# Performance work log

Measured on AMD Instinct MI355X. Metric: run time of the kernel, lower is better.

Reference implementation:

```python
import jax, jax.numpy as jnp
import numpy as np

D_MODEL = 2048
N_HEADS = 16
N_KV_HEADS = 4
HEAD_DIM = D_MODEL // N_HEADS  # 128
SWA_WINDOW = 1024
SINK_TOKENS = 4
ROPE_BASE = 10000.0
EPS = 1e-6


def setup_inputs() -> dict:
    key = jax.random.key(0)
    ks = jax.random.split(key, 6)
    s = 0.02
    B, T = 1, 4096
    return {
        "x": jax.random.normal(ks[0], (B, T, D_MODEL), dtype=jnp.float32),
        "wq": jax.random.normal(ks[1], (N_HEADS * HEAD_DIM, D_MODEL), dtype=jnp.float32) * s,
        "wk": jax.random.normal(ks[2], (N_KV_HEADS * HEAD_DIM, D_MODEL), dtype=jnp.float32) * s,
        "wv": jax.random.normal(ks[3], (N_KV_HEADS * HEAD_DIM, D_MODEL), dtype=jnp.float32) * s,
        "wo": jax.random.normal(ks[4], (D_MODEL, D_MODEL), dtype=jnp.float32) * s,
        "qk_weight": jnp.ones((HEAD_DIM,), dtype=jnp.float32),
        "layer_idx": 1,
    }


def _rope_cos_sin(T, dtype):
    half = HEAD_DIM // 2
    inv_freq = 1.0 / (ROPE_BASE ** (jnp.arange(half, dtype=dtype) / half))
    freqs = jnp.arange(T, dtype=dtype)[:, None] * inv_freq[None, :]  # [T, half]
    return jnp.cos(freqs), jnp.sin(freqs)


def _rot(x, cos, sin):
    # x: [B,H,T,D]; cos/sin: [T,D/2]
    half = HEAD_DIM // 2
    x1, x2 = x[..., :half], x[..., half:]
    return jnp.concatenate([x1 * cos - x2 * sin, x1 * sin + x2 * cos], axis=-1)


def _qknorm(x, w):
    rms = jnp.sqrt(jnp.mean(x * x, axis=-1, keepdims=True) + EPS)
    return x / rms * w


def reference(x, wq, wk, wv, wo, qk_weight, layer_idx):
    B, T, C = x.shape
    rep = N_HEADS // N_KV_HEADS
    q = (x @ wq.T).reshape(B, T, N_HEADS, HEAD_DIM).transpose(0, 2, 1, 3)      # [B,H,T,D]
    k = (x @ wk.T).reshape(B, T, N_KV_HEADS, HEAD_DIM).transpose(0, 2, 1, 3)   # [B,Hkv,T,D]
    v = (x @ wv.T).reshape(B, T, N_KV_HEADS, HEAD_DIM).transpose(0, 2, 1, 3)
    k = jnp.repeat(k, rep, axis=1)  # GQA expand, matches repeat_interleave
    v = jnp.repeat(v, rep, axis=1)

    cos, sin = _rope_cos_sin(T, x.dtype)
    q = _rot(q, cos, sin)
    k = _rot(k, cos, sin)

    q = _qknorm(q, qk_weight)
    k = _qknorm(k, qk_weight)

    # sliding-window + sink mask (non-global layer). NOTE: faithful to the
    # original, which passes ~allowed as the boolean keep-mask to SDPA.
    i = jnp.arange(T)[:, None]
    j = jnp.arange(T)[None, :]
    allowed = (j <= i) & (((i - j) < SWA_WINDOW) | (j < SINK_TOKENS))
    keep = ~allowed  # True = attend (SDPA bool-mask semantics)

    scale = HEAD_DIM ** -0.5
    scores = jnp.einsum('bhqd,bhkd->bhqk', q, k) * scale
    scores = jnp.where(keep[None, None], scores, -jnp.inf)
    attn = jax.nn.softmax(scores, axis=-1)
    y = jnp.einsum('bhqk,bhkd->bhqd', attn, v)
    y = y.transpose(0, 2, 1, 3).reshape(B, T, C)
    return y @ wo.T
```

## Files before the change

kernel.cpp:

```cpp
#include <hip/hip_runtime.h>

typedef unsigned short u16;
typedef __bf16 bf16x8_t __attribute__((ext_vector_type(8)));
typedef float f32x4 __attribute__((ext_vector_type(4)));
typedef u16 u16x8 __attribute__((ext_vector_type(8)));
typedef u16 u16x4 __attribute__((ext_vector_type(4)));

__device__ __forceinline__ u16 f2bf(float f) {
  union { float f; unsigned u; } v; v.f = f;
  unsigned r = v.u + 0x7FFFu + ((v.u >> 16) & 1u);
  return (u16)(r >> 16);
}
__device__ __forceinline__ float bf2f(u16 b) {
  union { unsigned u; float f; } v; v.u = ((unsigned)b) << 16;
  return v.f;
}
__device__ __forceinline__ f32x4 mfma_bf16(u16x8 a, u16x8 b, f32x4 c) {
  return __builtin_amdgcn_mfma_f32_16x16x32_bf16(
      __builtin_bit_cast(bf16x8_t, a), __builtin_bit_cast(bf16x8_t, b), c, 0, 0, 0);
}
__device__ __forceinline__ unsigned pack_bf16_trunc(float a, float b) {
  return __builtin_amdgcn_perm(__builtin_bit_cast(unsigned, b),
                               __builtin_bit_cast(unsigned, a), 0x07060302u);
}

__global__ void k_cvt_all(const float* __restrict__ x,  const float* __restrict__ wq,
                          const float* __restrict__ wk, const float* __restrict__ wv,
                          const float* __restrict__ wo, u16* __restrict__ xb,
                          u16* __restrict__ wqkvb, u16* __restrict__ wob) {
  const int i = blockIdx.x * blockDim.x + threadIdx.x;
  const float* src;
  u16* dst;
  int off;
  if (i < 2097152)      { src = x;  dst = xb;               off = i; }
  else if (i < 3145728) { src = wq; dst = wqkvb;            off = i - 2097152; }
  else if (i < 3407872) { src = wk; dst = wqkvb + 4194304;  off = i - 3145728; }
  else if (i < 3670016) { src = wv; dst = wqkvb + 5242880;  off = i - 3407872; }
  else                  { src = wo; dst = wob;              off = i - 3670016; }
  float4 v = reinterpret_cast<const float4*>(src)[off];
  u16x4 o = { f2bf(v.x), f2bf(v.y), f2bf(v.z), f2bf(v.w) };
  reinterpret_cast<u16x4*>(dst)[off] = o;
}

template<bool BF16OUT>
__global__ __launch_bounds__(256, 2)
void k_gemm_bt(const u16* __restrict__ A, const u16* __restrict__ B,
               void* __restrict__ Cv, int M, int N, int K) {
  __shared__ u16 lA[128 * 64];
  __shared__ u16 lB[128 * 64];
  const int bm = blockIdx.y, bn = blockIdx.x;
  const int tid = threadIdx.x;
  const int wid = tid >> 6, lane = tid & 63;
  const int lo = lane & 15, hi = lane >> 4;
  const int wrow = (wid >> 1) * 64, wcol = (wid & 1) * 64;
  f32x4 acc[4][4] = {};
  const size_t abase = (size_t)(bm * 128) * K;
  const size_t bbase = (size_t)(bn * 128) * K;
  for (int kt = 0; kt < K; kt += 64) {
#pragma unroll
    for (int rr = 0; rr < 4; ++rr) {
      int e = (rr * 256 + tid) * 8;
      int row = e >> 6, col = e & 63;
      u16x8 va = *reinterpret_cast<const u16x8*>(A + abase + (size_t)row * K + kt + col);
      u16x8 vb = *reinterpret_cast<const u16x8*>(B + bbase + (size_t)row * K + kt + col);
      int sw = ((row * 64 + col) * 2) ^ ((row & 7) << 4);
      *reinterpret_cast<u16x8*>(reinterpret_cast<char*>(lA) + sw) = va;
      *reinterpret_cast<u16x8*>(reinterpret_cast<char*>(lB) + sw) = vb;
    }
    __syncthreads();
#pragma unroll
    for (int ks = 0; ks < 64; ks += 32) {
      u16x8 af[4], bfr[4];
#pragma unroll
      for (int mi = 0; mi < 4; ++mi) {
        int row = wrow + mi * 16 + lo, col = ks + hi * 8;
        int sw = ((row * 64 + col) * 2) ^ ((row & 7) << 4);
        af[mi] = *reinterpret_cast<const u16x8*>(reinterpret_cast<char*>(lA) + sw);
      }
#pragma unroll
      for (int ni = 0; ni < 4; ++ni) {
        int row = wcol + ni * 16 + lo, col = ks + hi * 8;
        int sw = ((row * 64 + col) * 2) ^ ((row & 7) << 4);
        bfr[ni] = *reinterpret_cast<const u16x8*>(reinterpret_cast<char*>(lB) + sw);
      }
#pragma unroll
      for (int mi = 0; mi < 4; ++mi)
#pragma unroll
        for (int ni = 0; ni < 4; ++ni)
          acc[mi][ni] = mfma_bf16(af[mi], bfr[ni], acc[mi][ni]);
    }
    __syncthreads();
  }
#pragma unroll
  for (int mi = 0; mi < 4; ++mi)
#pragma unroll
    for (int ni = 0; ni < 4; ++ni)
#pragma unroll
      for (int r = 0; r < 4; ++r) {
        int row = bm * 128 + wrow + mi * 16 + hi * 4 + r;
        int col = bn * 128 + wcol + ni * 16 + lo;
        if (BF16OUT)
          ((u16*)Cv)[(size_t)row * N + col] = f2bf(acc[mi][ni][r]);
        else
          ((float*)Cv)[(size_t)row * N + col] = acc[mi][ni][r];
      }
}

#define ATT_SL2E 0.12754276432973518f
__global__ void k_rope_norm(const u16* __restrict__ QKV, const float* __restrict__ qkw,
                            u16* __restrict__ qb, u16* __restrict__ kb) {
  int gw = blockIdx.x * 4 + (threadIdx.x >> 6);
  int lane = threadIdx.x & 63;
  int t = gw / 20, hh = gw - t * 20;
  const u16* src = QKV + (size_t)t * 3072 + (hh < 16 ? hh * 128 : 2048 + (hh - 16) * 128);
  float x1 = bf2f(src[lane]), x2 = bf2f(src[lane + 64]);
  float invf = exp2f(-(float)lane * (13.287712379549449f / 64.0f));
  float fr = (float)t * invf;
  float sn, cs;
  sincosf(fr, &sn, &cs);
  float o1 = x1 * cs - x2 * sn, o2 = x1 * sn + x2 * cs;
  float ss = o1 * o1 + o2 * o2;
#pragma unroll
  for (int off = 32; off > 0; off >>= 1) ss += __shfl_xor(ss, off);
  float inv = rsqrtf(ss * (1.0f / 128.0f) + 1e-6f);
  inv *= (hh < 16) ? ATT_SL2E : 1.0f;
  o1 *= inv * qkw[lane];
  o2 *= inv * qkw[lane + 64];
  u16* dst = (hh < 16) ? (qb + ((size_t)hh * 4096 + t) * 128)
                       : (kb + ((size_t)(hh - 16) * 4096 + t) * 128);
  dst[lane] = f2bf(o1);
  dst[lane + 64] = f2bf(o2);
}

__global__ void k_transpose_v(const u16* __restrict__ QKV, u16* __restrict__ vtb) {
  __shared__ float lt[64][65];
  int b = blockIdx.x;
  int dt = b & 1, tt = (b >> 1) & 63, kv = b >> 7;
  int tid = threadIdx.x;
#pragma unroll
  for (int rr = 0; rr < 16; ++rr) {
    int row = rr * 4 + (tid >> 6);
    int col = tid & 63;
    lt[row][col] = bf2f(QKV[(size_t)(tt * 64 + row) * 3072 + 2560 + kv * 128 + dt * 64 + col]);
  }
  __syncthreads();
#pragma unroll
  for (int pp = 0; pp < 2; ++pp) {
    int idx = pp * 256 + tid;
    int dr = idx >> 3, tc = (idx & 7) * 8;
    const int grp = tc >> 5;
    const int pb = tc & 31;
    u16x8 o;
#pragma unroll
    for (int i = 0; i < 8; ++i) {
      const int p = pb + i;
      const int g = (p & 3) | (((p >> 3) & 3) << 2) | (((p >> 2) & 1) << 4);
      o[i] = f2bf(lt[grp * 32 + g][dr]);
    }
    *reinterpret_cast<u16x8*>(vtb + (size_t)(kv * 128 + dt * 64 + dr) * 4096 + tt * 64 + tc) = o;
  }
}

#define KPAD 136
#define VPAD 40

__global__ __launch_bounds__(256)
void k_attn_mfma(const u16* __restrict__ qb, const u16* __restrict__ kb,
                 const u16* __restrict__ vtb, u16* __restrict__ yb) {
  __shared__ u16 sK[2][32][KPAD];
  __shared__ u16 sV[2][128][VPAD];
  const int id = blockIdx.x;
  const int work = (id & 7) * 64 + (id >> 3);
  const int kvh = work >> 7;
  const int rem = work & 127;
  const int h = kvh * 4 + (rem >> 5);
  const int qt = rem & 31;
  const int tid = threadIdx.x;
  const int wid = tid >> 6, lane = tid & 63;
  const int lo = lane & 15, hi = lane >> 4;
  const int q0 = qt * 128;
  const int qwA = q0 + wid * 16;
  const int qwB = qwA + 64;
  const int qrowA = qwA + lo, qrowB = qwB + lo;
  const u16* qpA = qb + ((size_t)h * 4096 + qrowA) * 128;
  const u16* qpB = qb + ((size_t)h * 4096 + qrowB) * 128;
  u16x8 qfA[4], qfB[4];
#pragma unroll
  for (int dc = 0; dc < 4; ++dc) {
    qfA[dc] = *reinterpret_cast<const u16x8*>(qpA + dc * 32 + hi * 8);
    qfB[dc] = *reinterpret_cast<const u16x8*>(qpB + dc * 32 + hi * 8);
  }
  f32x4 accOA[8] = {}, accOB[8] = {};
  float lsA = 0.0f, lsB = 0.0f;
  const u16* kbase = kb + (size_t)kvh * 4096 * 128;
  const u16* vb = vtb + (size_t)kvh * 128 * 4096;

  int past_tiles = 0;
  const int pe = q0 + 127 - 1024;
  if (pe >= 4) past_tiles = (pe >> 5) + 1;
  const int fstart = (q0 + 1) >> 5;
  const int ntiles = past_tiles + (128 - fstart);
  const int safe_past_hi = (q0 >= 1056) ? ((q0 - 1055) >> 5) : 0;
  const int funmask = (q0 >> 5) + 4;

  u16x8 kr[2], vr[2];
#define STAGE_LOAD(KT)                                                          \
  {                                                                             \
    const int kt_ = (KT);                                                       \
    _Pragma("unroll")                                                           \
    for (int p = 0; p < 2; ++p) {                                               \
      const int c = tid + p * 256;                                              \
      kr[p] = *reinterpret_cast<const u16x8*>(                                  \
          kbase + (size_t)(kt_ * 32 + (c >> 4)) * 128 + (c & 15) * 8);          \
      vr[p] = *reinterpret_cast<const u16x8*>(                                  \
          vb + (size_t)(c >> 2) * 4096 + kt_ * 32 + (c & 3) * 8);               \
    }                                                                           \
  }
#define STAGE_WRITE(BUF)                                                        \
  {                                                                             \
    const int b_ = (BUF);                                                       \
    _Pragma("unroll")                                                           \
    for (int p = 0; p < 2; ++p) {                                               \
      const int c = tid + p * 256;                                              \
      *reinterpret_cast<u16x8*>(&sK[b_][c >> 4][(c & 15) * 8]) = kr[p];         \
      *reinterpret_cast<u16x8*>(&sV[b_][c >> 2][(c & 3) * 8]) = vr[p];          \
    }                                                                           \
  }
#define COMPUTE(MSK)                                                            \
  {                                                                             \
    f32x4 aSA[2] = {}, aSB[2] = {};                                             \
    __builtin_amdgcn_s_setprio(1);                                              \
    _Pragma("unroll")                                                           \
    for (int sub = 0; sub < 2; ++sub)                                           \
      _Pragma("unroll")                                                         \
      for (int dc = 0; dc < 4; ++dc) {                                          \
        u16x8 kf = *reinterpret_cast<const u16x8*>(                             \
            &sK[cur][sub * 16 + lo][dc * 32 + hi * 8]);                         \
        aSA[sub] = mfma_bf16(kf, qfA[dc], aSA[sub]);                            \
        aSB[sub] = mfma_bf16(kf, qfB[dc], aSB[sub]);                            \
      }                                                                         \
    __builtin_amdgcn_s_setprio(0);                                              \
    unsigned wA[4], wB[4];                                                      \
    _Pragma("unroll")                                                           \
    for (int sub = 0; sub < 2; ++sub) {                                         \
      float eA[4], eB[4];                                                       \
      _Pragma("unroll")                                                         \
      for (int r = 0; r < 4; ++r) {                                             \
        float pA = exp2f(aSA[sub][r]);                                          \
        float pB = exp2f(aSB[sub][r]);                                          \
        if (MSK) {                                                              \
          const int j = kt * 32 + sub * 16 + hi * 4 + r;                        \
          const bool okA = (j > qrowA) || (((qrowA - j) >= 1024) && (j >= 4));  \
          const bool okB = (j > qrowB) || (((qrowB - j) >= 1024) && (j >= 4));  \
          pA = okA ? pA : 0.0f;                                                 \
          pB = okB ? pB : 0.0f;                                                 \
        }                                                                       \
        lsA += pA; lsB += pB;                                                   \
        eA[r] = pA; eB[r] = pB;                                                 \
      }                                                                         \
      wA[sub * 2]     = pack_bf16_trunc(eA[0], eA[1]);                          \
      wA[sub * 2 + 1] = pack_bf16_trunc(eA[2], eA[3]);                          \
      wB[sub * 2]     = pack_bf16_trunc(eB[0], eB[1]);                          \
      wB[sub * 2 + 1] = pack_bf16_trunc(eB[2], eB[3]);                          \
    }                                                                           \
    uint4 tA4 = { wA[0], wA[1], wA[2], wA[3] };                                 \
    uint4 tB4 = { wB[0], wB[1], wB[2], wB[3] };                                 \
    u16x8 pfA = __builtin_bit_cast(u16x8, tA4);                                 \
    u16x8 pfB = __builtin_bit_cast(u16x8, tB4);                                 \
    __builtin_amdgcn_s_setprio(1);                                              \
    _Pragma("unroll")                                                           \
    for (int nt = 0; nt < 8; ++nt) {                                            \
      u16x8 vf = *reinterpret_cast<const u16x8*>(&sV[cur][nt * 16 + lo][hi * 8]); \
      accOA[nt] = mfma_bf16(pfA, vf, accOA[nt]);                                \
      accOB[nt] = mfma_bf16(pfB, vf, accOB[nt]);                                \
    }                                                                           \
    __builtin_amdgcn_s_setprio(0);                                              \
  }

  STAGE_LOAD(0 < past_tiles ? 0 : fstart);
  STAGE_WRITE(0);
  __syncthreads();

  for (int i = 0; i < ntiles; ++i) {
    const int cur = i & 1;
    const int kt = (i < past_tiles) ? i : fstart + (i - past_tiles);
    const bool more = (i + 1) < ntiles;
    if (more) {
      const int i1 = i + 1;
      STAGE_LOAD((i1 < past_tiles) ? i1 : fstart + (i1 - past_tiles));
    }
    const bool msk = (i < past_tiles) ? ((kt == 0) || (kt > safe_past_hi))
                                      : (kt < funmask);
    if (msk) COMPUTE(true) else COMPUTE(false);
    if (more) STAGE_WRITE(cur ^ 1);
    __syncthreads();
  }
#undef STAGE_LOAD
#undef STAGE_WRITE
#undef COMPUTE

  lsA += __shfl_xor(lsA, 16); lsA += __shfl_xor(lsA, 32);
  lsB += __shfl_xor(lsB, 16); lsB += __shfl_xor(lsB, 32);
  float lrA[4], lrB[4];
#pragma unroll
  for (int r = 0; r < 4; ++r) {
    lrA[r] = 1.0f / __shfl(lsA, hi * 4 + r);
    lrB[r] = 1.0f / __shfl(lsB, hi * 4 + r);
  }
#pragma unroll
  for (int nt = 0; nt < 8; ++nt)
#pragma unroll
    for (int r = 0; r < 4; ++r) {
      const int tA = qwA + hi * 4 + r;
      const int tB = qwB + hi * 4 + r;
      yb[(size_t)tA * 2048 + h * 128 + nt * 16 + lo] = f2bf(accOA[nt][r] * lrA[r]);
      yb[(size_t)tB * 2048 + h * 128 + nt * 16 + lo] = f2bf(accOB[nt][r] * lrB[r]);
    }
}

extern "C" void kernel_launch(void* const* d_in, const int* in_sizes, int n_in,
                              void* d_out, int out_size, void* d_ws, size_t ws_size,
                              hipStream_t stream) {
  const float* x   = (const float*)d_in[0];
  const float* wq  = (const float*)d_in[1];
  const float* wk  = (const float*)d_in[2];
  const float* wv  = (const float*)d_in[3];
  const float* wo  = (const float*)d_in[4];
  const float* qkw = (const float*)d_in[5];
  (void)in_sizes; (void)n_in; (void)out_size; (void)ws_size;

  char* ws = (char*)d_ws;
  u16* xb    = (u16*)(ws);
  u16* wqkvb = (u16*)(ws + (16ull << 20));
  u16* wob   = (u16*)(ws + (28ull << 20));
  u16* qkvb  = (u16*)(ws + (36ull << 20));
  u16* qb    = (u16*)(ws + (60ull << 20));
  u16* kb    = (u16*)(ws + (76ull << 20));
  u16* vtb   = (u16*)(ws + (80ull << 20));
  u16* yb    = (u16*)(ws + (84ull << 20));

  k_cvt_all<<<18432, 256, 0, stream>>>(x, wq, wk, wv, wo, xb, wqkvb, wob);
  k_gemm_bt<true><<<dim3(24, 32), 256, 0, stream>>>(xb, wqkvb, qkvb, 4096, 3072, 2048);
  k_rope_norm<<<20480, 256, 0, stream>>>(qkvb, qkw, qb, kb);
  k_transpose_v<<<512, 256, 0, stream>>>(qkvb, vtb);
  k_attn_mfma<<<512, 256, 0, stream>>>(qb, kb, vtb, yb);
  k_gemm_bt<false><<<dim3(16, 32), 256, 0, stream>>>(yb, wob, (float*)d_out, 4096, 2048, 2048);
}
```

Measured before the change: 336.6 us.

## Software-pipeline attention loop: overlap next tile's QK MFMA with previous softmax and PV

Restructures the attention tile loop so that each iteration computes QK scores for the current tile and then runs exp2, masking and the PV MFMAs for the previous tile. Scores and V fragments are carried across iterations in registers (sSA/sSB, vfp), with a prologue and a final FINISH epilogue. The aim is to let the transcendental and softmax VALU work overlap with matrix-core work and to hide the LDS latency of the V reads. In exchange it adds register pressure from the eight held V fragments and the carried score accumulators, which could lower occupancy or cause spills.

```diff
diff --git a/kernel.cpp b/kernel.cpp
--- a/kernel.cpp
+++ b/kernel.cpp
@@ -203,6 +203,14 @@
   const int safe_past_hi = (q0 >= 1056) ? ((q0 - 1055) >> 5) : 0;
   const int funmask = (q0 >> 5) + 4;
 
+#define KT_OF(i) (((i) < past_tiles) ? (i) : (fstart + ((i) - past_tiles)))
+#define MSK_OF(i, ktv) (((i) < past_tiles) ? (((ktv) == 0) || ((ktv) > safe_past_hi)) \
+                                           : ((ktv) < funmask))
+
+  f32x4 sSA[2], sSB[2];
+  u16x8 vfp[8];
+  int ktP = 0, mskP = 0;
+
   u16x8 kr[2], vr[2];
 #define STAGE_LOAD(KT)                                                          \
   {                                                                             \
@@ -226,30 +234,32 @@
       *reinterpret_cast<u16x8*>(&sV[b_][c >> 2][(c & 3) * 8]) = vr[p];          \
     }                                                                           \
   }
-#define COMPUTE(MSK)                                                            \
-  {                                                                             \
-    f32x4 aSA[2] = {}, aSB[2] = {};                                             \
+#define QK_PHASE(CUR)                                                           \
     __builtin_amdgcn_s_setprio(1);                                              \
     _Pragma("unroll")                                                           \
     for (int sub = 0; sub < 2; ++sub)                                           \
       _Pragma("unroll")                                                         \
       for (int dc = 0; dc < 4; ++dc) {                                          \
         u16x8 kf = *reinterpret_cast<const u16x8*>(                             \
-            &sK[cur][sub * 16 + lo][dc * 32 + hi * 8]);                         \
-        aSA[sub] = mfma_bf16(kf, qfA[dc], aSA[sub]);                            \
-        aSB[sub] = mfma_bf16(kf, qfB[dc], aSB[sub]);                            \
+            &sK[CUR][sub * 16 + lo][dc * 32 + hi * 8]);                         \
+        nSA[sub] = mfma_bf16(kf, qfA[dc], nSA[sub]);                            \
+        nSB[sub] = mfma_bf16(kf, qfB[dc], nSB[sub]);                            \
       }                                                                         \
-    __builtin_amdgcn_s_setprio(0);                                              \
-    unsigned wA[4], wB[4];                                                      \
+    __builtin_amdgcn_s_setprio(0);
+#define VF_LOAD(CUR)                                                            \
+    _Pragma("unroll")                                                           \
+    for (int nt = 0; nt < 8; ++nt)                                              \
+      vfp[nt] = *reinterpret_cast<const u16x8*>(&sV[CUR][nt * 16 + lo][hi * 8]);
+#define SOFT(MSKLIT)                                                            \
     _Pragma("unroll")                                                           \
     for (int sub = 0; sub < 2; ++sub) {                                         \
       float eA[4], eB[4];                                                       \
       _Pragma("unroll")                                                         \
       for (int r = 0; r < 4; ++r) {                                             \
-        float pA = exp2f(aSA[sub][r]);                                          \
-        float pB = exp2f(aSB[sub][r]);                                          \
-        if (MSK) {                                                              \
-          const int j = kt * 32 + sub * 16 + hi * 4 + r;                        \
+        float pA = exp2f(sSA[sub][r]);                                          \
+        float pB = exp2f(sSB[sub][r]);                                          \
+        if (MSKLIT) {                                                           \
+          const int j = ktP * 32 + sub * 16 + hi * 4 + r;                       \
           const bool okA = (j > qrowA) || (((qrowA - j) >= 1024) && (j >= 4));  \
           const bool okB = (j > qrowB) || (((qrowB - j) >= 1024) && (j >= 4));  \
           pA = okA ? pA : 0.0f;                                                 \
@@ -262,7 +272,11 @@
       wA[sub * 2 + 1] = pack_bf16_trunc(eA[2], eA[3]);                          \
       wB[sub * 2]     = pack_bf16_trunc(eB[0], eB[1]);                          \
       wB[sub * 2 + 1] = pack_bf16_trunc(eB[2], eB[3]);                          \
-    }                                                                           \
+    }
+#define FINISH()                                                                \
+  {                                                                             \
+    unsigned wA[4], wB[4];                                                      \
+    if (mskP) { SOFT(true) } else { SOFT(false) }                               \
     uint4 tA4 = { wA[0], wA[1], wA[2], wA[3] };                                 \
     uint4 tB4 = { wB[0], wB[1], wB[2], wB[3] };                                 \
     u16x8 pfA = __builtin_bit_cast(u16x8, tA4);                                 \
@@ -270,34 +284,54 @@
     __builtin_amdgcn_s_setprio(1);                                              \
     _Pragma("unroll")                                                           \
     for (int nt = 0; nt < 8; ++nt) {                                            \
-      u16x8 vf = *reinterpret_cast<const u16x8*>(&sV[cur][nt * 16 + lo][hi * 8]); \
-      accOA[nt] = mfma_bf16(pfA, vf, accOA[nt]);                                \
-      accOB[nt] = mfma_bf16(pfB, vf, accOB[nt]);                                \
+      accOA[nt] = mfma_bf16(pfA, vfp[nt], accOA[nt]);                           \
+      accOB[nt] = mfma_bf16(pfB, vfp[nt], accOB[nt]);                           \
     }                                                                           \
     __builtin_amdgcn_s_setprio(0);                                              \
   }
 
-  STAGE_LOAD(0 < past_tiles ? 0 : fstart);
+  STAGE_LOAD(KT_OF(0));
   STAGE_WRITE(0);
   __syncthreads();
-
-  for (int i = 0; i < ntiles; ++i) {
+  {
+    if (ntiles > 1) STAGE_LOAD(KT_OF(1));
+    f32x4 nSA[2] = {}, nSB[2] = {};
+    QK_PHASE(0);
+    VF_LOAD(0);
+    sSA[0] = nSA[0]; sSA[1] = nSA[1];
+    sSB[0] = nSB[0]; sSB[1] = nSB[1];
+    ktP = KT_OF(0);
+    mskP = MSK_OF(0, ktP) ? 1 : 0;
+    if (ntiles > 1) STAGE_WRITE(1);
+    __syncthreads();
+  }
+  for (int i = 1; i < ntiles; ++i) {
     const int cur = i & 1;
-    const int kt = (i < past_tiles) ? i : fstart + (i - past_tiles);
     const bool more = (i + 1) < ntiles;
-    if (more) {
-      const int i1 = i + 1;
-      STAGE_LOAD((i1 < past_tiles) ? i1 : fstart + (i1 - past_tiles));
-    }
-    const bool msk = (i < past_tiles) ? ((kt == 0) || (kt > safe_past_hi))
-                                      : (kt < funmask);
-    if (msk) COMPUTE(true) else COMPUTE(false);
+    if (more) STAGE_LOAD(KT_OF(i + 1));
+    f32x4 nSA[2] = {}, nSB[2] = {};
+    QK_PHASE(cur);
+    FINISH();
+    VF_LOAD(cur);
+    sSA[0] = nSA[0]; sSA[1] = nSA[1];
+    sSB[0] = nSB[0]; sSB[1] = nSB[1];
+    {
+      const int ktc = KT_OF(i);
+      ktP = ktc;
+      mskP = MSK_OF(i, ktc) ? 1 : 0;
+    }
     if (more) STAGE_WRITE(cur ^ 1);
     __syncthreads();
   }
+  FINISH();
 #undef STAGE_LOAD
 #undef STAGE_WRITE
-#undef COMPUTE
+#undef QK_PHASE
+#undef VF_LOAD
+#undef SOFT
+#undef FINISH
+#undef KT_OF
+#undef MSK_OF
 
   lsA += __shfl_xor(lsA, 16); lsA += __shfl_xor(lsA, 32);
   lsB += __shfl_xor(lsB, 16); lsB += __shfl_xor(lsB, 32);
```

Result: faster. 310.4 us (-7.8%).
